# Optimization experiments

Measured on AMD Instinct MI355X. Metric: run time of the kernel, lower is better.

Reference implementation:

```python
import jax, jax.numpy as jnp
import numpy as np

B_BATCH, N_ATOMS, N_CGS = 128, 512, 16


def setup_inputs() -> dict:
    key = jax.random.key(0)
    k0, k1, k2, k3, k4, k5 = jax.random.split(key, 6)
    npair = N_CGS * N_CGS
    soft_assign = jax.random.uniform(k0, (B_BATCH, N_ATOMS, N_CGS), dtype=jnp.float32)
    a = jax.random.uniform(k1, (B_BATCH, N_ATOMS, N_CGS), dtype=jnp.float32)
    assign_norm = a / a.sum(axis=-1, keepdims=True)  # row-normalized soft assignment
    xyz = jax.random.normal(k2, (B_BATCH, N_ATOMS, 3), dtype=jnp.float32)
    cg_xyz = jax.random.normal(k3, (B_BATCH, N_CGS, 3), dtype=jnp.float32)
    W = 0.01 * jax.random.normal(k4, (N_ATOMS, npair + npair * npair), dtype=jnp.float32)
    assign_idx = jax.random.randint(k5, (N_ATOMS,), 0, N_CGS)
    return {"soft_assign": soft_assign, "xyz": xyz, "cg_xyz": cg_xyz,
            "assign_norm": assign_norm, "W": W, "assign_idx": assign_idx}


def reference(soft_assign, xyz, cg_xyz, assign_norm, W, assign_idx):
    b, n_cgs = cg_xyz.shape[0], cg_xyz.shape[1]
    npair = n_cgs * n_cgs
    # pairwise displacement basis: basis[b,i,j] = cg_xyz[b,j] - cg_xyz[b,i]
    basis = cg_xyz[:, None, :, :] - cg_xyz[:, :, None, :]      # [b, nc, nc, 3]
    Bmat = basis.reshape(b, npair, 3)                          # [b, npair, 3]
    # cross basis: entry (p,q) = cross(Bmat[q], Bmat[p]) (matches torch Bij x Bjk)
    cross_basis = jnp.cross(Bmat[:, None, :, :], Bmat[:, :, None, :])  # [b,npair,npair,3]
    Bfull = jnp.concatenate([Bmat, cross_basis.reshape(b, npair * npair, 3)], axis=1)
    # dx_recon[b,n,e] = sum_j Bfull[b,j,e] * W[n,j]
    dx_recon = jnp.einsum('bje,nj->bne', Bfull, W)             # [b, n_atoms, 3]
    # per-CG mean offset weighted by soft assignment
    cg_offset = jnp.einsum('bin,bij->bjn', dx_recon, assign_norm)  # [b, n_cgs, 3]
    xyz_recon = cg_xyz[:, assign_idx, :] - cg_offset[:, assign_idx, :] + dx_recon
    return (soft_assign, xyz, xyz_recon)
```

## Files before the change

kernel.cpp:

```cpp
#include <hip/hip_runtime.h>

constexpr int NC = 16;
constexpr int NP = 256;
constexpr int PITCH = 264;
constexpr int NATOMS = 512;
constexpr int NB = 128;
constexpr int WROW = NP + NP * NP;
constexpr int ANP = 21;
constexpr int DXP = 5;

__global__ __launch_bounds__(256) void k_stream(const float* __restrict__ W,
                                                const float* __restrict__ soft_assign,
                                                const float* __restrict__ xyz,
                                                float* __restrict__ wcd_part,
                                                float* __restrict__ w1c,
                                                float* __restrict__ out_sa,
                                                float* __restrict__ out_xyz) {
    __shared__ float Hl[NC][PITCH];
    const int bid = blockIdx.x;
    const int n = bid >> 1;
    const int half = bid & 1;
    const int t = threadIdx.x;

    ((float4*)out_sa)[bid * 256 + t] = ((const float4*)soft_assign)[bid * 256 + t];
    if (t < 48) {
        ((float4*)out_xyz)[bid * 48 + t] = ((const float4*)xyz)[bid * 48 + t];
    }

    if (half == 0 && t < NC) {
        const float* __restrict__ W1 = W + (size_t)n * WROW;
        float a1 = 0.f;
#pragma unroll
        for (int pi = 0; pi < NC; ++pi) a1 += W1[pi * NC + t];
#pragma unroll
        for (int pj = 0; pj < NC; ++pj) a1 -= W1[t * NC + pj];
        w1c[n * NC + t] = a1;
    }

    const float* __restrict__ wp =
        W + (size_t)n * WROW + NP + (size_t)(half * 128) * NP + t;
    float h[NC];
#pragma unroll
    for (int d = 0; d < NC; ++d) h[d] = 0.f;
    float hn[8];
#pragma unroll
    for (int g = 0; g < 8; ++g) {
        float s = 0.f;
#pragma unroll
        for (int i = 0; i < 16; ++i) {
            const float v = wp[(size_t)(g * 16 + i) * NP];
            h[i] += v;
            s += v;
        }
        hn[g] = s;
    }
    if (half == 0) {
        h[0] -= hn[0]; h[1] -= hn[1]; h[2] -= hn[2]; h[3] -= hn[3];
        h[4] -= hn[4]; h[5] -= hn[5]; h[6] -= hn[6]; h[7] -= hn[7];
    } else {
        h[8]  -= hn[0]; h[9]  -= hn[1]; h[10] -= hn[2]; h[11] -= hn[3];
        h[12] -= hn[4]; h[13] -= hn[5]; h[14] -= hn[6]; h[15] -= hn[7];
    }

#pragma unroll
    for (int d = 0; d < NC; ++d) Hl[d][t] = h[d];
    __syncthreads();

    {
        const int d = t >> 4, c = t & 15;
        float rp = 0.f, rm = 0.f;
#pragma unroll
        for (int qi = 0; qi < NC; ++qi) rp += Hl[d][qi * NC + c];
#pragma unroll
        for (int qj = 0; qj < NC; ++qj) rm += Hl[d][c * NC + qj];
        wcd_part[((size_t)half * NATOMS + n) * NP + t] = rp - rm;
    }
}

__global__ __launch_bounds__(256) void k_dx(const float* __restrict__ cg_xyz,
                                            const float* __restrict__ wcd_part,
                                            const float* __restrict__ w1c,
                                            float* __restrict__ dxp) {
    __shared__ float xs[NC][4];
    __shared__ float cxs[64][4];
    const int b = blockIdx.x >> 2;
    const int q = blockIdx.x & 3;
    const int t = threadIdx.x;

    if (t < 48) xs[t / 3][t % 3] = cg_xyz[(size_t)b * NC * 3 + t];
    __syncthreads();
    if (t < 64) {
        const int m = q * 64 + t, c = m & 15, d = m >> 4;
        const float ax = xs[c][0], ay = xs[c][1], az = xs[c][2];
        const float bx = xs[d][0], by = xs[d][1], bz = xs[d][2];
        cxs[t][0] = ay * bz - az * by;
        cxs[t][1] = az * bx - ax * bz;
        cxs[t][2] = ax * by - ay * bx;
        cxs[t][3] = 0.f;
    }
    __syncthreads();

#pragma unroll
    for (int a = 0; a < 2; ++a) {
        const int n = a * 256 + t;
        const float4* __restrict__ w0 =
            (const float4*)(wcd_part + (size_t)n * NP + q * 64);
        const float4* __restrict__ w1 =
            (const float4*)(wcd_part + ((size_t)NATOMS + n) * NP + q * 64);
        float dx0 = 0.f, dx1 = 0.f, dx2 = 0.f;
#pragma unroll
        for (int k4 = 0; k4 < 16; ++k4) {
            const float4 wa = w0[k4];
            const float4 wb = w1[k4];
            float4 w;
            w.x = wa.x + wb.x; w.y = wa.y + wb.y;
            w.z = wa.z + wb.z; w.w = wa.w + wb.w;
            const float4 c0 = *(const float4*)(&cxs[k4 * 4 + 0][0]);
            const float4 c1 = *(const float4*)(&cxs[k4 * 4 + 1][0]);
            const float4 c2 = *(const float4*)(&cxs[k4 * 4 + 2][0]);
            const float4 c3 = *(const float4*)(&cxs[k4 * 4 + 3][0]);
            dx0 += w.x * c0.x + w.y * c1.x + w.z * c2.x + w.w * c3.x;
            dx1 += w.x * c0.y + w.y * c1.y + w.z * c2.y + w.w * c3.y;
            dx2 += w.x * c0.z + w.y * c1.z + w.z * c2.z + w.w * c3.z;
        }
        if (q == 0) {
            const float* __restrict__ w1r = w1c + n * NC;
#pragma unroll
            for (int c = 0; c < NC; ++c) {
                const float wv = w1r[c];
                dx0 += wv * xs[c][0]; dx1 += wv * xs[c][1]; dx2 += wv * xs[c][2];
            }
        }
        float* __restrict__ op = dxp + (((size_t)q * NB + b) * NATOMS + n) * 3;
        op[0] = dx0; op[1] = dx1; op[2] = dx2;
    }
}

__global__ __launch_bounds__(512) void k_finish(const float* __restrict__ cg_xyz,
                                                const float* __restrict__ assign_norm,
                                                const int* __restrict__ assign_idx,
                                                const float* __restrict__ dxp,
                                                float* __restrict__ out_recon) {
    __shared__ float an_l[NATOMS][ANP];
    __shared__ float dxl[NATOMS][DXP];
    __shared__ float xs[NC][4];
    __shared__ float cgo_l[NC][4];
    const int b = blockIdx.x;
    const int t = threadIdx.x;

    {
        const float4* __restrict__ anr =
            (const float4*)(assign_norm + ((size_t)b * NATOMS + t) * NC);
#pragma unroll
        for (int i = 0; i < 4; ++i) {
            const float4 v = anr[i];
            an_l[t][4 * i + 0] = v.x; an_l[t][4 * i + 1] = v.y;
            an_l[t][4 * i + 2] = v.z; an_l[t][4 * i + 3] = v.w;
        }
    }
    if (t < 48) xs[t / 3][t % 3] = cg_xyz[(size_t)b * NC * 3 + t];

    float dx0, dx1, dx2;
    {
        const size_t s0 = (((size_t)0 * NB + b) * NATOMS + t) * 3;
        const size_t s1 = (((size_t)1 * NB + b) * NATOMS + t) * 3;
        const size_t s2 = (((size_t)2 * NB + b) * NATOMS + t) * 3;
        const size_t s3 = (((size_t)3 * NB + b) * NATOMS + t) * 3;
        dx0 = (dxp[s0 + 0] + dxp[s1 + 0]) + (dxp[s2 + 0] + dxp[s3 + 0]);
        dx1 = (dxp[s0 + 1] + dxp[s1 + 1]) + (dxp[s2 + 1] + dxp[s3 + 1]);
        dx2 = (dxp[s0 + 2] + dxp[s1 + 2]) + (dxp[s2 + 2] + dxp[s3 + 2]);
    }
    dxl[t][0] = dx0; dxl[t][1] = dx1; dxl[t][2] = dx2;
    __syncthreads();

    {
        const int j = t >> 5, g = t & 31;
        float p0 = 0.f, p1 = 0.f, p2 = 0.f;
#pragma unroll
        for (int k = 0; k < 16; ++k) {
            const int i = g + 32 * k;
            const float a = an_l[i][j];
            p0 += a * dxl[i][0];
            p1 += a * dxl[i][1];
            p2 += a * dxl[i][2];
        }
#pragma unroll
        for (int s = 1; s < 32; s <<= 1) {
            p0 += __shfl_xor(p0, s);
            p1 += __shfl_xor(p1, s);
            p2 += __shfl_xor(p2, s);
        }
        if (g == 0) { cgo_l[j][0] = p0; cgo_l[j][1] = p1; cgo_l[j][2] = p2; }
    }
    __syncthreads();

    const int ci = assign_idx[t];
    const float r0 = xs[ci][0] - cgo_l[ci][0] + dx0;
    const float r1 = xs[ci][1] - cgo_l[ci][1] + dx1;
    const float r2 = xs[ci][2] - cgo_l[ci][2] + dx2;
    const size_t ob = ((size_t)b * NATOMS + t) * 3;
    out_recon[ob + 0] = r0;
    out_recon[ob + 1] = r1;
    out_recon[ob + 2] = r2;
}

extern "C" void kernel_launch(void* const* d_in, const int* in_sizes, int n_in,
                              void* d_out, int out_size, void* d_ws, size_t ws_size,
                              hipStream_t stream) {
    (void)in_sizes; (void)n_in; (void)out_size; (void)ws_size;
    const float* soft_assign = (const float*)d_in[0];
    const float* xyz         = (const float*)d_in[1];
    const float* cg_xyz      = (const float*)d_in[2];
    const float* assign_norm = (const float*)d_in[3];
    const float* W           = (const float*)d_in[4];
    const int*   assign_idx  = (const int*)d_in[5];

    float* out       = (float*)d_out;
    float* out_sa    = out;
    float* out_xyz   = out + (size_t)NB * NATOMS * NC;
    float* out_recon = out_xyz + (size_t)NB * NATOMS * 3;

    float* wcd_part = (float*)d_ws;
    float* w1c      = wcd_part + (size_t)2 * NATOMS * NP;
    float* dxp      = w1c + (size_t)NATOMS * NC;

    k_stream<<<dim3(NATOMS * 2), dim3(256), 0, stream>>>(W, soft_assign, xyz,
                                                         wcd_part, w1c,
                                                         out_sa, out_xyz);
    k_dx<<<dim3(NB * 4), dim3(256), 0, stream>>>(cg_xyz, wcd_part, w1c, dxp);
    k_finish<<<dim3(NB), dim3(512), 0, stream>>>(cg_xyz, assign_norm, assign_idx,
                                                 dxp, out_recon);
}
```

Measured before the change: 52.74 us.

## Use one block per atom with float4 W streaming and in-block partial reduction

k_stream now launches one block per atom instead of two half-blocks. Each thread streams W with float4 loads over 64 rows, and the four 64-thread slices reduce their partial H accumulators through shared memory. Because a full wcd row is written per atom, k_dx no longer reads and adds two partial buffers, which cuts workspace traffic. In exchange the grid is half as large, registers rise (sixteen float4 accumulators) and shared memory use is four times larger, so occupancy for the bandwidth-bound W stream may drop.

Result: faster. 44.80 us (median of 2 runs) (-15.1%).

```diff
diff --git a/kernel.cpp b/kernel.cpp
--- a/kernel.cpp
+++ b/kernel.cpp
@@ -9,25 +9,28 @@
 constexpr int ANP = 21;
 constexpr int DXP = 5;
 
+#define F4ADD(a, v) do { (a).x += (v).x; (a).y += (v).y; (a).z += (v).z; (a).w += (v).w; } while (0)
+#define F4SUB(a, v) do { (a).x -= (v).x; (a).y -= (v).y; (a).z -= (v).z; (a).w -= (v).w; } while (0)
+
 __global__ __launch_bounds__(256) void k_stream(const float* __restrict__ W,
                                                 const float* __restrict__ soft_assign,
                                                 const float* __restrict__ xyz,
-                                                float* __restrict__ wcd_part,
+                                                float* __restrict__ wcd,
                                                 float* __restrict__ w1c,
                                                 float* __restrict__ out_sa,
                                                 float* __restrict__ out_xyz) {
-    __shared__ float Hl[NC][PITCH];
-    const int bid = blockIdx.x;
-    const int n = bid >> 1;
-    const int half = bid & 1;
+    __shared__ float Hp[4][NC][PITCH];
+    const int n = blockIdx.x;
     const int t = threadIdx.x;
-
-    ((float4*)out_sa)[bid * 256 + t] = ((const float4*)soft_assign)[bid * 256 + t];
-    if (t < 48) {
-        ((float4*)out_xyz)[bid * 48 + t] = ((const float4*)xyz)[bid * 48 + t];
-    }
-
-    if (half == 0 && t < NC) {
+    const int s = t >> 6;
+    const int l = t & 63;
+
+    ((float4*)out_sa)[n * 512 + t]       = ((const float4*)soft_assign)[n * 512 + t];
+    ((float4*)out_sa)[n * 512 + 256 + t] = ((const float4*)soft_assign)[n * 512 + 256 + t];
+    if (t < 96) {
+        ((float4*)out_xyz)[n * 96 + t] = ((const float4*)xyz)[n * 96 + t];
+    }
+    if (t < NC) {
         const float* __restrict__ W1 = W + (size_t)n * WROW;
         float a1 = 0.f;
 #pragma unroll
@@ -37,48 +40,62 @@
         w1c[n * NC + t] = a1;
     }
 
-    const float* __restrict__ wp =
-        W + (size_t)n * WROW + NP + (size_t)(half * 128) * NP + t;
-    float h[NC];
-#pragma unroll
-    for (int d = 0; d < NC; ++d) h[d] = 0.f;
-    float hn[8];
-#pragma unroll
-    for (int g = 0; g < 8; ++g) {
-        float s = 0.f;
-#pragma unroll
-        for (int i = 0; i < 16; ++i) {
-            const float v = wp[(size_t)(g * 16 + i) * NP];
-            h[i] += v;
-            s += v;
-        }
-        hn[g] = s;
-    }
-    if (half == 0) {
-        h[0] -= hn[0]; h[1] -= hn[1]; h[2] -= hn[2]; h[3] -= hn[3];
-        h[4] -= hn[4]; h[5] -= hn[5]; h[6] -= hn[6]; h[7] -= hn[7];
-    } else {
-        h[8]  -= hn[0]; h[9]  -= hn[1]; h[10] -= hn[2]; h[11] -= hn[3];
-        h[12] -= hn[4]; h[13] -= hn[5]; h[14] -= hn[6]; h[15] -= hn[7];
-    }
-
-#pragma unroll
-    for (int d = 0; d < NC; ++d) Hl[d][t] = h[d];
+    const float4* __restrict__ wp =
+        (const float4*)W + ((size_t)n * 16448 + 64 + (size_t)(s * 64) * 64 + l);
+    float4 h4[NC], hn4[4];
+#pragma unroll
+    for (int d = 0; d < NC; ++d) { h4[d].x = 0.f; h4[d].y = 0.f; h4[d].z = 0.f; h4[d].w = 0.f; }
+#pragma unroll
+    for (int g = 0; g < 4; ++g) { hn4[g].x = 0.f; hn4[g].y = 0.f; hn4[g].z = 0.f; hn4[g].w = 0.f; }
+#pragma unroll
+    for (int i = 0; i < 64; ++i) {
+        const float4 v = wp[(size_t)i * 64];
+        F4ADD(h4[i & 15], v);
+        F4ADD(hn4[i >> 4], v);
+    }
+    switch (s) {
+      case 0:
+#pragma unroll
+        for (int k = 0; k < 4; ++k) F4SUB(h4[k], hn4[k]);
+        break;
+      case 1:
+#pragma unroll
+        for (int k = 0; k < 4; ++k) F4SUB(h4[4 + k], hn4[k]);
+        break;
+      case 2:
+#pragma unroll
+        for (int k = 0; k < 4; ++k) F4SUB(h4[8 + k], hn4[k]);
+        break;
+      default:
+#pragma unroll
+        for (int k = 0; k < 4; ++k) F4SUB(h4[12 + k], hn4[k]);
+        break;
+    }
+#pragma unroll
+    for (int d = 0; d < NC; ++d) {
+        *(float4*)(&Hp[s][d][4 * l]) = h4[d];
+    }
+    __syncthreads();
+
+#pragma unroll
+    for (int d = 0; d < NC; ++d) {
+        Hp[0][d][t] += (Hp[1][d][t] + Hp[2][d][t]) + Hp[3][d][t];
+    }
     __syncthreads();
 
     {
         const int d = t >> 4, c = t & 15;
         float rp = 0.f, rm = 0.f;
 #pragma unroll
-        for (int qi = 0; qi < NC; ++qi) rp += Hl[d][qi * NC + c];
-#pragma unroll
-        for (int qj = 0; qj < NC; ++qj) rm += Hl[d][c * NC + qj];
-        wcd_part[((size_t)half * NATOMS + n) * NP + t] = rp - rm;
+        for (int qi = 0; qi < NC; ++qi) rp += Hp[0][d][qi * NC + c];
+#pragma unroll
+        for (int qj = 0; qj < NC; ++qj) rm += Hp[0][d][c * NC + qj];
+        wcd[n * NP + t] = rp - rm;
     }
 }
 
 __global__ __launch_bounds__(256) void k_dx(const float* __restrict__ cg_xyz,
-                                            const float* __restrict__ wcd_part,
+                                            const float* __restrict__ wcd,
                                             const float* __restrict__ w1c,
                                             float* __restrict__ dxp) {
     __shared__ float xs[NC][4];
@@ -104,17 +121,11 @@
     for (int a = 0; a < 2; ++a) {
         const int n = a * 256 + t;
         const float4* __restrict__ w0 =
-            (const float4*)(wcd_part + (size_t)n * NP + q * 64);
-        const float4* __restrict__ w1 =
-            (const float4*)(wcd_part + ((size_t)NATOMS + n) * NP + q * 64);
+            (const float4*)(wcd + (size_t)n * NP + q * 64);
         float dx0 = 0.f, dx1 = 0.f, dx2 = 0.f;
 #pragma unroll
         for (int k4 = 0; k4 < 16; ++k4) {
-            const float4 wa = w0[k4];
-            const float4 wb = w1[k4];
-            float4 w;
-            w.x = wa.x + wb.x; w.y = wa.y + wb.y;
-            w.z = wa.z + wb.z; w.w = wa.w + wb.w;
+            const float4 w = w0[k4];
             const float4 c0 = *(const float4*)(&cxs[k4 * 4 + 0][0]);
             const float4 c1 = *(const float4*)(&cxs[k4 * 4 + 1][0]);
             const float4 c2 = *(const float4*)(&cxs[k4 * 4 + 2][0]);
@@ -185,10 +196,10 @@
             p2 += a * dxl[i][2];
         }
 #pragma unroll
-        for (int s = 1; s < 32; s <<= 1) {
-            p0 += __shfl_xor(p0, s);
-            p1 += __shfl_xor(p1, s);
-            p2 += __shfl_xor(p2, s);
+        for (int sh = 1; sh < 32; sh <<= 1) {
+            p0 += __shfl_xor(p0, sh);
+            p1 += __shfl_xor(p1, sh);
+            p2 += __shfl_xor(p2, sh);
         }
         if (g == 0) { cgo_l[j][0] = p0; cgo_l[j][1] = p1; cgo_l[j][2] = p2; }
     }
@@ -220,14 +231,13 @@
     float* out_xyz   = out + (size_t)NB * NATOMS * NC;
     float* out_recon = out_xyz + (size_t)NB * NATOMS * 3;
 
-    float* wcd_part = (float*)d_ws;
-    float* w1c      = wcd_part + (size_t)2 * NATOMS * NP;
-    float* dxp      = w1c + (size_t)NATOMS * NC;
-
-    k_stream<<<dim3(NATOMS * 2), dim3(256), 0, stream>>>(W, soft_assign, xyz,
-                                                         wcd_part, w1c,
-                                                         out_sa, out_xyz);
-    k_dx<<<dim3(NB * 4), dim3(256), 0, stream>>>(cg_xyz, wcd_part, w1c, dxp);
+    float* wcd = (float*)d_ws;
+    float* w1c = wcd + (size_t)NATOMS * NP;
+    float* dxp = w1c + (size_t)NATOMS * NC;
+
+    k_stream<<<dim3(NATOMS), dim3(256), 0, stream>>>(W, soft_assign, xyz,
+                                                     wcd, w1c, out_sa, out_xyz);
+    k_dx<<<dim3(NB * 4), dim3(256), 0, stream>>>(cg_xyz, wcd, w1c, dxp);
     k_finish<<<dim3(NB), dim3(512), 0, stream>>>(cg_xyz, assign_norm, assign_idx,
                                                  dxp, out_recon);
 }
```
